# Kernel optimization log

Hardware: AMD Instinct MI355X
Metric: run time of the kernel (lower is better)

The kernel has to match this reference:

```python
import jax, jax.numpy as jnp
import numpy as np

N_NODES = 20000
N_EDGES = 256000
DIM = 128
N_LAYERS = 4


def _bn(x, gamma, beta, eps=1e-5):
    # BatchNorm1d in training mode: batch statistics over the node/edge axis
    mu = x.mean(0)
    var = ((x - mu) ** 2).mean(0)
    return gamma * (x - mu) * jax.lax.rsqrt(var + eps) + beta


def setup_inputs() -> dict:
    key = jax.random.key(0)
    ks = jax.random.split(key, 32)
    s = 1.0 / np.sqrt(DIM)
    inp = {
        'h': jax.random.normal(ks[0], (N_NODES, DIM), jnp.float32),
        'e': jax.random.normal(ks[1], (N_EDGES, DIM), jnp.float32),
        'src': jax.random.randint(ks[2], (N_EDGES,), 0, N_NODES, jnp.int32),
        'dst': jax.random.randint(ks[3], (N_EDGES,), 0, N_NODES, jnp.int32),
        'W_emb_h': jax.random.normal(ks[4], (DIM, DIM), jnp.float32) * s,
        'b_emb_h': jnp.zeros((DIM,), jnp.float32),
        'W_emb_e': jax.random.normal(ks[5], (DIM, DIM), jnp.float32) * s,
        'b_emb_e': jnp.zeros((DIM,), jnp.float32),
    }
    for i, nm in enumerate(['A', 'B', 'C', 'D', 'E']):
        inp[nm + 'w'] = jax.random.normal(ks[6 + i], (N_LAYERS, DIM, DIM), jnp.float32) * s
        inp[nm + 'b'] = jnp.zeros((N_LAYERS, DIM), jnp.float32)
    inp['gh'] = jnp.ones((N_LAYERS, DIM), jnp.float32)
    inp['bh'] = jnp.zeros((N_LAYERS, DIM), jnp.float32)
    inp['ge'] = jnp.ones((N_LAYERS, DIM), jnp.float32)
    inp['be'] = jnp.zeros((N_LAYERS, DIM), jnp.float32)
    return inp


def reference(h, e, src, dst, W_emb_h, b_emb_h, W_emb_e, b_emb_e,
              Aw, Ab, Bw, Bb, Cw, Cb, Dw, Db, Ew, Eb, gh, bh, ge, be):
    n_nodes = h.shape[0]
    # input embeddings
    h = h @ W_emb_h + b_emb_h
    e = e @ W_emb_e + b_emb_e
    for l in range(Aw.shape[0]):
        h_in, e_in = h, e
        Ah = h @ Aw[l] + Ab[l]
        Bh = h @ Bw[l] + Bb[l]
        Dh = h @ Dw[l] + Db[l]
        Eh = h @ Ew[l] + Eb[l]
        Ce = e @ Cw[l] + Cb[l]
        # edge gates: e_ij = D h_i + E h_j + C e_ij  (edge i->j)
        e_new = Dh[src] + Eh[dst] + Ce            # [E, D]
        sigma = jax.nn.sigmoid(e_new)
        num = jax.ops.segment_sum(sigma * Bh[src], dst, num_segments=n_nodes)
        den = jax.ops.segment_sum(sigma, dst, num_segments=n_nodes)
        h_new = Ah + num / (den + 1e-6)
        h_new = _bn(h_new, gh[l], bh[l])
        e_new = _bn(e_new, ge[l], be[l])
        # relu + residual (dropout = 0)
        h = h_in + jax.nn.relu(h_new)
        e = e_in + jax.nn.relu(e_new)
    return h
```

## Files before the change

kernel.cpp:

```cpp
#include <hip/hip_runtime.h>
#include <hip/hip_bf16.h>

typedef __attribute__((ext_vector_type(8))) short short8;
typedef __attribute__((ext_vector_type(4))) float floatx4;
typedef __attribute__((ext_vector_type(4))) unsigned short ushortx4;

__device__ __forceinline__ float bf2f(unsigned short u) {
    union { float f; unsigned int i; } v; v.i = ((unsigned int)u) << 16; return v.f;
}
__device__ __forceinline__ unsigned short f2bf(float f) {
    union { float f; unsigned int i; } v; v.f = f;
    unsigned int r = v.i + 0x7fffu + ((v.i >> 16) & 1u);
    return (unsigned short)(r >> 16);
}

__global__ void deg_count(const int* __restrict__ dst, int* __restrict__ deg, int E) {
    int i = blockIdx.x * 256 + threadIdx.x;
    if (i < E) atomicAdd(&deg[dst[i]], 1);
}

__global__ __launch_bounds__(1024) void scan_rowptr(const int* __restrict__ deg,
                                                    int* __restrict__ rowptr,
                                                    int* __restrict__ cursor, int N) {
    const int CH = 20;
    __shared__ int buf[1024];
    int t = threadIdx.x;
    int base = t * CH;
    int local[CH];
    int tot = 0;
#pragma unroll
    for (int k = 0; k < CH; ++k) {
        int i = base + k;
        int v = (i < N) ? deg[i] : 0;
        local[k] = tot;
        tot += v;
    }
    buf[t] = tot;
    __syncthreads();
    for (int off = 1; off < 1024; off <<= 1) {
        int x = (t >= off) ? buf[t - off] : 0;
        __syncthreads();
        buf[t] += x;
        __syncthreads();
    }
    int excl = buf[t] - tot;
#pragma unroll
    for (int k = 0; k < CH; ++k) {
        int i = base + k;
        if (i < N) { rowptr[i] = excl + local[k]; cursor[i] = excl + local[k]; }
    }
    if (t == 1023) rowptr[N] = buf[1023];
}

__global__ void scatter_edges(const int* __restrict__ src, const int* __restrict__ dst,
                              int* __restrict__ cursor, int* __restrict__ eix,
                              int* __restrict__ sx, int E) {
    int i = blockIdx.x * 256 + threadIdx.x;
    if (i >= E) return;
    int d = dst[i];
    int pos = atomicAdd(&cursor[d], 1);
    eix[pos] = i;
    sx[pos] = src[i];
}

__global__ void transpose_w(const float* __restrict__ Wh,
                            const float* __restrict__ We,
                            const float* __restrict__ Aw,
                            const float* __restrict__ Bw,
                            const float* __restrict__ Cw,
                            const float* __restrict__ Dw,
                            const float* __restrict__ Ew,
                            unsigned short* __restrict__ Wt) {
    int i = blockIdx.x * 256 + threadIdx.x;
    const int total = 22 * 16384;
    if (i >= total) return;
    int slot = i >> 14;
    int r = i & 16383;
    int n = r >> 7;
    int k = r & 127;
    const float* srcp;
    if (slot == 0) srcp = Wh;
    else if (slot == 1) srcp = We;
    else {
        int t = slot - 2;
        int l = t / 5, w = t % 5;
        const float* bases[5] = {Aw, Bw, Cw, Dw, Ew};
        srcp = bases[w] + l * 16384;
    }
    Wt[i] = f2bf(srcp[k * 128 + n]);
}

template <int IN_BF16, int OUT_BF16, int GATHER>
__global__ __launch_bounds__(256) void gemm128(const void* __restrict__ Ain,
                                               const int* __restrict__ ridx,
                                               const unsigned short* __restrict__ Wt,
                                               const float* __restrict__ bias,
                                               void* __restrict__ Cout, int nStrips) {
    const int lane = threadIdx.x & 63;
    const int wv = threadIdx.x >> 6;
    const int m16 = lane & 15;
    const int kg = lane >> 4;

    short8 b[4][2];
#pragma unroll
    for (int j = 0; j < 2; ++j)
#pragma unroll
        for (int ks = 0; ks < 4; ++ks)
            b[ks][j] = *(const short8*)(Wt + ((wv * 2 + j) * 16 + m16) * 128 + ks * 32 + kg * 8);

    floatx4 bv[2];
#pragma unroll
    for (int j = 0; j < 2; ++j)
        bv[j] = *(const floatx4*)(bias + (wv * 2 + j) * 16 + kg * 4);

    const float* Af = (const float*)Ain;
    const unsigned short* Ab16 = (const unsigned short*)Ain;

    const int stride = gridDim.x;
    int s0 = blockIdx.x;
    if (s0 >= nStrips) return;

    auto loadA = [&](int s, short8* a) {
        int rowA = s * 16 + m16;
        if (GATHER) rowA = ridx[rowA];
        size_t rowBase = (size_t)rowA * 128;
#pragma unroll
        for (int ks = 0; ks < 4; ++ks) {
            int off = ks * 32 + kg * 8;
            if (IN_BF16) {
                a[ks] = *(const short8*)(Ab16 + rowBase + off);
            } else {
                floatx4 f0 = *(const floatx4*)(Af + rowBase + off);
                floatx4 f1 = *(const floatx4*)(Af + rowBase + off + 4);
                short8 t;
                t[0] = (short)f2bf(f0[0]); t[1] = (short)f2bf(f0[1]);
                t[2] = (short)f2bf(f0[2]); t[3] = (short)f2bf(f0[3]);
                t[4] = (short)f2bf(f1[0]); t[5] = (short)f2bf(f1[1]);
                t[6] = (short)f2bf(f1[2]); t[7] = (short)f2bf(f1[3]);
                a[ks] = t;
            }
        }
    };

    short8 a0[4], a1[4];
    loadA(s0, a0);
    for (int s = s0; s < nStrips; s += stride) {
        int sn = s + stride;
        if (sn < nStrips) loadA(sn, a1);

        floatx4 acc[2];
        acc[0] = (floatx4){0.f, 0.f, 0.f, 0.f};
        acc[1] = (floatx4){0.f, 0.f, 0.f, 0.f};
#pragma unroll
        for (int ks = 0; ks < 4; ++ks) {
            acc[0] = __builtin_amdgcn_mfma_f32_16x16x32_bf16(b[ks][0], a0[ks], acc[0], 0, 0, 0);
            acc[1] = __builtin_amdgcn_mfma_f32_16x16x32_bf16(b[ks][1], a0[ks], acc[1], 0, 0, 0);
        }

        size_t rbase = ((size_t)s * 16 + m16) * 128;
#pragma unroll
        for (int j = 0; j < 2; ++j) {
            int c0 = (wv * 2 + j) * 16 + kg * 4;
            if (OUT_BF16) {
                ushortx4 o;
#pragma unroll
                for (int i = 0; i < 4; ++i) o[i] = f2bf(acc[j][i] + bv[j][i]);
                *(ushortx4*)((unsigned short*)Cout + rbase + c0) = o;
            } else {
                floatx4 o;
#pragma unroll
                for (int i = 0; i < 4; ++i) o[i] = acc[j][i] + bv[j][i];
                *(floatx4*)((float*)Cout + rbase + c0) = o;
            }
        }
#pragma unroll
        for (int ks = 0; ks < 4; ++ks) a0[ks] = a1[ks];
    }
}

__global__ __launch_bounds__(1024) void gemm_h4(const float* __restrict__ h_cur,
                                                const unsigned short* __restrict__ WtL,
                                                const float* __restrict__ Abi,
                                                const float* __restrict__ Bbi,
                                                const float* __restrict__ Dbi,
                                                const float* __restrict__ Ebi,
                                                float* __restrict__ AhB,
                                                unsigned short* __restrict__ BD16,
                                                unsigned short* __restrict__ Eh16,
                                                int nStrips) {
    const int lane = threadIdx.x & 63;
    const int w = threadIdx.x >> 6;
    const int m16 = lane & 15;
    const int kg = lane >> 4;

    short8 bf[4][2];
    floatx4 bv[2];
    if (w < 8) {
        const int slot = (w < 4) ? 0 : 4;
        const float* bp = (w < 4) ? Abi : Ebi;
        const int ntb = (w & 3) * 2;
#pragma unroll
        for (int j = 0; j < 2; ++j) {
#pragma unroll
            for (int ks = 0; ks < 4; ++ks)
                bf[ks][j] = *(const short8*)(WtL + slot * 16384 +
                                             ((ntb + j) * 16 + m16) * 128 + ks * 32 + kg * 8);
            bv[j] = *(const floatx4*)(bp + (ntb + j) * 16 + kg * 4);
        }
    } else {
        const int nt = w - 8;
#pragma unroll
        for (int ks = 0; ks < 4; ++ks) {
            bf[ks][0] = *(const short8*)(WtL + 1 * 16384 + (nt * 16 + m16) * 128 + ks * 32 + kg * 8);
            bf[ks][1] = *(const short8*)(WtL + 3 * 16384 + (nt * 16 + m16) * 128 + ks * 32 + kg * 8);
        }
        bv[0] = *(const floatx4*)(Bbi + nt * 16 + kg * 4);
        bv[1] = *(const floatx4*)(Dbi + nt * 16 + kg * 4);
    }

    for (int s = blockIdx.x; s < nStrips; s += gridDim.x) {
        size_t rowBase = ((size_t)s * 16 + m16) * 128;
        short8 a[4];
#pragma unroll
        for (int ks = 0; ks < 4; ++ks) {
            int off = ks * 32 + kg * 8;
            floatx4 f0 = *(const floatx4*)(h_cur + rowBase + off);
            floatx4 f1 = *(const floatx4*)(h_cur + rowBase + off + 4);
            short8 t;
            t[0] = (short)f2bf(f0[0]); t[1] = (short)f2bf(f0[1]);
            t[2] = (short)f2bf(f0[2]); t[3] = (short)f2bf(f0[3]);
            t[4] = (short)f2bf(f1[0]); t[5] = (short)f2bf(f1[1]);
            t[6] = (short)f2bf(f1[2]); t[7] = (short)f2bf(f1[3]);
            a[ks] = t;
        }

        floatx4 acc0 = (floatx4){0.f, 0.f, 0.f, 0.f};
        floatx4 acc1 = (floatx4){0.f, 0.f, 0.f, 0.f};
#pragma unroll
        for (int ks = 0; ks < 4; ++ks) {
            acc0 = __builtin_amdgcn_mfma_f32_16x16x32_bf16(bf[ks][0], a[ks], acc0, 0, 0, 0);
            acc1 = __builtin_amdgcn_mfma_f32_16x16x32_bf16(bf[ks][1], a[ks], acc1, 0, 0, 0);
        }

        size_t r = (size_t)s * 16 + m16;
        if (w < 4) {
            const int ntb = (w & 3) * 2;
            floatx4 o0, o1;
#pragma unroll
            for (int i = 0; i < 4; ++i) { o0[i] = acc0[i] + bv[0][i]; o1[i] = acc1[i] + bv[1][i]; }
            *(floatx4*)(AhB + r * 128 + (ntb + 0) * 16 + kg * 4) = o0;
            *(floatx4*)(AhB + r * 128 + (ntb + 1) * 16 + kg * 4) = o1;
        } else if (w < 8) {
            const int ntb = (w & 3) * 2;
            ushortx4 o0, o1;
#pragma unroll
            for (int i = 0; i < 4; ++i) {
                o0[i] = f2bf(acc0[i] + bv[0][i]);
                o1[i] = f2bf(acc1[i] + bv[1][i]);
            }
            *(ushortx4*)(Eh16 + r * 128 + (ntb + 0) * 16 + kg * 4) = o0;
            *(ushortx4*)(Eh16 + r * 128 + (ntb + 1) * 16 + kg * 4) = o1;
        } else {
            const int nt = w - 8;
            short8 o;
#pragma unroll
            for (int i = 0; i < 4; ++i) {
                o[2 * i]     = (short)f2bf(acc0[i] + bv[0][i]);
                o[2 * i + 1] = (short)f2bf(acc1[i] + bv[1][i]);
            }
            *(short8*)(BD16 + r * 256 + (nt * 16 + kg * 4) * 2) = o;
        }
    }
}

template <int DO_E>
__global__ __launch_bounds__(256) void node_aggregate(unsigned short* __restrict__ Ce,
                                                      const unsigned short* __restrict__ BD16,
                                                      const unsigned short* __restrict__ Eh16,
                                                      const int* __restrict__ rowptr,
                                                      const int* __restrict__ sx,
                                                      const float* __restrict__ Ah,
                                                      float* __restrict__ h_new,
                                                      float* __restrict__ sums, int N) {
    const int q = threadIdx.x & 31;
    const int g = threadIdx.x >> 5;
    float hs[4] = {0.f, 0.f, 0.f, 0.f};
    float hq[4] = {0.f, 0.f, 0.f, 0.f};
    float es[4] = {0.f, 0.f, 0.f, 0.f};
    float eq[4] = {0.f, 0.f, 0.f, 0.f};
    for (int d = blockIdx.x * 8 + g; d < N; d += gridDim.x * 8) {
        int beg = rowptr[d], end = rowptr[d + 1];
        ushortx4 eh4 = *(const ushortx4*)(Eh16 + (size_t)d * 128 + q * 4);
        float ehf[4];
#pragma unroll
        for (int k = 0; k < 4; ++k) ehf[k] = bf2f(eh4[k]);
        float num[4] = {0.f, 0.f, 0.f, 0.f};
        float den[4] = {0.f, 0.f, 0.f, 0.f};
        int j = beg;
        for (; j + 1 < end; j += 2) {
            int s0 = sx[j], s1 = sx[j + 1];
            ushortx4 c0 = *(const ushortx4*)(Ce + (size_t)j * 128 + q * 4);
            ushortx4 c1 = *(const ushortx4*)(Ce + (size_t)(j + 1) * 128 + q * 4);
            short8 bd0 = *(const short8*)(BD16 + (size_t)s0 * 256 + q * 8);
            short8 bd1 = *(const short8*)(BD16 + (size_t)s1 * 256 + q * 8);
            ushortx4 o0, o1;
#pragma unroll
            for (int k = 0; k < 4; ++k) {
                float en0 = bf2f(c0[k]) + bf2f((unsigned short)bd0[2 * k + 1]) + ehf[k];
                float en1 = bf2f(c1[k]) + bf2f((unsigned short)bd1[2 * k + 1]) + ehf[k];
                if (DO_E) {
                    es[k] += en0 + en1;
                    eq[k] += en0 * en0 + en1 * en1;
                    o0[k] = f2bf(en0);
                    o1[k] = f2bf(en1);
                }
                float sg0 = 1.f / (1.f + __expf(-en0));
                float sg1 = 1.f / (1.f + __expf(-en1));
                den[k] += sg0 + sg1;
                num[k] += sg0 * bf2f((unsigned short)bd0[2 * k])
                        + sg1 * bf2f((unsigned short)bd1[2 * k]);
            }
            if (DO_E) {
                *(ushortx4*)(Ce + (size_t)j * 128 + q * 4) = o0;
                *(ushortx4*)(Ce + (size_t)(j + 1) * 128 + q * 4) = o1;
            }
        }
        if (j < end) {
            int s0 = sx[j];
            ushortx4 c0 = *(const ushortx4*)(Ce + (size_t)j * 128 + q * 4);
            short8 bd0 = *(const short8*)(BD16 + (size_t)s0 * 256 + q * 8);
            ushortx4 o0;
#pragma unroll
            for (int k = 0; k < 4; ++k) {
                float en0 = bf2f(c0[k]) + bf2f((unsigned short)bd0[2 * k + 1]) + ehf[k];
                if (DO_E) {
                    es[k] += en0;
                    eq[k] += en0 * en0;
                    o0[k] = f2bf(en0);
                }
                float sg0 = 1.f / (1.f + __expf(-en0));
                den[k] += sg0;
                num[k] += sg0 * bf2f((unsigned short)bd0[2 * k]);
            }
            if (DO_E) *(ushortx4*)(Ce + (size_t)j * 128 + q * 4) = o0;
        }
        floatx4 ah = *(const floatx4*)(Ah + (size_t)d * 128 + q * 4);
        floatx4 out;
#pragma unroll
        for (int k = 0; k < 4; ++k) {
            float v = ah[k] + num[k] / (den[k] + 1e-6f);
            out[k] = v;
            hs[k] += v;
            hq[k] += v * v;
        }
        *(floatx4*)(h_new + (size_t)d * 128 + q * 4) = out;
    }
    __shared__ float ls[512];
    ls[threadIdx.x] = 0.f;
    ls[256 + threadIdx.x] = 0.f;
    __syncthreads();
#pragma unroll
    for (int k = 0; k < 4; ++k) {
        atomicAdd(&ls[q * 4 + k], hs[k]);
        atomicAdd(&ls[128 + q * 4 + k], hq[k]);
        if (DO_E) {
            atomicAdd(&ls[256 + q * 4 + k], es[k]);
            atomicAdd(&ls[384 + q * 4 + k], eq[k]);
        }
    }
    __syncthreads();
    atomicAdd(&sums[threadIdx.x], ls[threadIdx.x]);
    if (DO_E) atomicAdd(&sums[256 + threadIdx.x], ls[256 + threadIdx.x]);
}

__global__ void finalize_stats(const float* __restrict__ sums,
                               const float* __restrict__ gh,
                               const float* __restrict__ bh,
                               const float* __restrict__ ge,
                               const float* __restrict__ be,
                               float* __restrict__ coef, int N, int E) {
    int c = threadIdx.x;
    if (c >= 128) return;
    float muh = sums[c] / (float)N;
    float vh = fmaxf(sums[128 + c] / (float)N - muh * muh, 0.f);
    float rsh = rsqrtf(vh + 1e-5f);
    float g = gh[c], bt = bh[c];
    coef[c] = g * rsh;
    coef[128 + c] = bt - g * rsh * muh;
    float mue = sums[256 + c] / (float)E;
    float ve = fmaxf(sums[384 + c] / (float)E - mue * mue, 0.f);
    float rse = rsqrtf(ve + 1e-5f);
    float g2 = ge[c], b2 = be[c];
    coef[256 + c] = g2 * rse;
    coef[384 + c] = b2 - g2 * rse * mue;
}

__global__ __launch_bounds__(256) void h_update(const float* __restrict__ h_new,
                                                const float* __restrict__ coef,
                                                float* __restrict__ h_cur,
                                                float* __restrict__ out, int N) {
    const int c = threadIdx.x & 127;
    float sa = coef[c], sb = coef[128 + c];
    int total = N * 128;
    for (int i = blockIdx.x * blockDim.x + threadIdx.x; i < total; i += gridDim.x * blockDim.x) {
        float v = h_new[i] * sa + sb;
        v = v > 0.f ? v : 0.f;
        float h = h_cur[i] + v;
        h_cur[i] = h;
        if (out) out[i] = h;
    }
}

__global__ __launch_bounds__(256) void e_update(const unsigned short* __restrict__ e_new,
                                                const float* __restrict__ coef,
                                                unsigned short* __restrict__ e_cur, int E) {
    int total8 = E * 16;
    for (int idx = blockIdx.x * blockDim.x + threadIdx.x; idx < total8;
         idx += gridDim.x * blockDim.x) {
        int c8 = (idx & 15) * 8;
        short8 en = *(const short8*)(e_new + (size_t)idx * 8);
        short8 ec = *(const short8*)(e_cur + (size_t)idx * 8);
        floatx4 sa0 = *(const floatx4*)(coef + 256 + c8);
        floatx4 sa1 = *(const floatx4*)(coef + 256 + c8 + 4);
        floatx4 sb0 = *(const floatx4*)(coef + 384 + c8);
        floatx4 sb1 = *(const floatx4*)(coef + 384 + c8 + 4);
        short8 r;
#pragma unroll
        for (int k = 0; k < 8; ++k) {
            float sa = (k < 4) ? sa0[k] : sa1[k - 4];
            float sb = (k < 4) ? sb0[k] : sb1[k - 4];
            float v = bf2f((unsigned short)en[k]) * sa + sb;
            v = v > 0.f ? v : 0.f;
            r[k] = (short)f2bf(bf2f((unsigned short)ec[k]) + v);
        }
        *(short8*)(e_cur + (size_t)idx * 8) = r;
    }
}

extern "C" void kernel_launch(void* const* d_in, const int* in_sizes, int n_in,
                              void* d_out, int out_size, void* d_ws, size_t ws_size,
                              hipStream_t stream) {
    const int N = 20000, E = 256000, L = 4;

    const float* h_in = (const float*)d_in[0];
    const float* e_in = (const float*)d_in[1];
    const int* src = (const int*)d_in[2];
    const int* dst = (const int*)d_in[3];
    const float* Wemb_h = (const float*)d_in[4];
    const float* bemb_h = (const float*)d_in[5];
    const float* Wemb_e = (const float*)d_in[6];
    const float* bemb_e = (const float*)d_in[7];
    const float* Aw = (const float*)d_in[8];
    const float* Abi = (const float*)d_in[9];
    const float* Bw = (const float*)d_in[10];
    const float* Bbi = (const float*)d_in[11];
    const float* Cw = (const float*)d_in[12];
    const float* Cbi = (const float*)d_in[13];
    const float* Dw = (const float*)d_in[14];
    const float* Dbi = (const float*)d_in[15];
    const float* Ew = (const float*)d_in[16];
    const float* Ebi = (const float*)d_in[17];
    const float* gh = (const float*)d_in[18];
    const float* bh = (const float*)d_in[19];
    const float* ge = (const float*)d_in[20];
    const float* be = (const float*)d_in[21];

    char* p = (char*)d_ws;
    auto carve = [&](size_t bytes) {
        void* r = (void*)p;
        p += ((bytes + 255) & ~(size_t)255);
        return r;
    };
    unsigned short* Wt = (unsigned short*)carve((size_t)22 * 16384 * 2);
    float* h_cur = (float*)carve((size_t)N * 128 * 4);
    unsigned short* e_cur = (unsigned short*)carve((size_t)E * 128 * 2);
    unsigned short* e_new = (unsigned short*)carve((size_t)E * 128 * 2);
    float* AhB = (float*)carve((size_t)N * 128 * 4);
    unsigned short* BD16 = (unsigned short*)carve((size_t)N * 256 * 2);
    unsigned short* Eh16 = (unsigned short*)carve((size_t)N * 128 * 2);
    float* h_newB = (float*)carve((size_t)N * 128 * 4);
    float* sums = (float*)carve(4 * 128 * 4);
    float* coef = (float*)carve(4 * 128 * 4);
    int* deg = (int*)carve((size_t)N * 4);
    int* rowptr = (int*)carve((size_t)(N + 1) * 4);
    int* cursor = (int*)carve((size_t)N * 4);
    int* eix = (int*)carve((size_t)E * 4);
    int* sx = (int*)carve((size_t)E * 4);

    hipMemsetAsync(deg, 0, (size_t)N * 4, stream);
    deg_count<<<(E + 255) / 256, 256, 0, stream>>>(dst, deg, E);
    scan_rowptr<<<1, 1024, 0, stream>>>(deg, rowptr, cursor, N);
    scatter_edges<<<(E + 255) / 256, 256, 0, stream>>>(src, dst, cursor, eix, sx, E);

    transpose_w<<<(22 * 16384 + 255) / 256, 256, 0, stream>>>(Wemb_h, Wemb_e, Aw, Bw, Cw, Dw, Ew, Wt);

    gemm128<0, 0, 0><<<1024, 256, 0, stream>>>(h_in, nullptr, Wt + 0 * 16384, bemb_h, h_cur, N / 16);
    gemm128<0, 1, 1><<<1024, 256, 0, stream>>>(e_in, eix, Wt + 1 * 16384, bemb_e, e_cur, E / 16);

    for (int l = 0; l < L; ++l) {
        int last = (l == L - 1);
        hipMemsetAsync(sums, 0, 4 * 128 * 4, stream);
        const unsigned short* WtL = Wt + (size_t)(2 + l * 5) * 16384;
        gemm_h4<<<250, 1024, 0, stream>>>(h_cur, WtL, Abi + l * 128, Bbi + l * 128,
                                          Dbi + l * 128, Ebi + l * 128, AhB, BD16, Eh16,
                                          N / 16);
        gemm128<1, 1, 0><<<1024, 256, 0, stream>>>(e_cur, nullptr, WtL + 2 * 16384, Cbi + l * 128,
                                                   e_new, E / 16);
        if (!last)
            node_aggregate<1><<<1250, 256, 0, stream>>>(e_new, BD16, Eh16, rowptr, sx, AhB,
                                                        h_newB, sums, N);
        else
            node_aggregate<0><<<1250, 256, 0, stream>>>(e_new, BD16, Eh16, rowptr, sx, AhB,
                                                        h_newB, sums, N);
        finalize_stats<<<1, 128, 0, stream>>>(sums, gh + l * 128, bh + l * 128, ge + l * 128,
                                              be + l * 128, coef, N, E);
        h_update<<<512, 256, 0, stream>>>(h_newB, coef, h_cur, last ? (float*)d_out : nullptr, N);
        if (!last) e_update<<<2048, 256, 0, stream>>>(e_new, coef, e_cur, E);
    }
}
```

Before: 1.061 ms.

## Stage GEMM A tiles into LDS via async global_load_lds double buffering

```diff
diff --git a/kernel.cpp b/kernel.cpp
--- a/kernel.cpp
+++ b/kernel.cpp
@@ -4,6 +4,9 @@
 typedef __attribute__((ext_vector_type(8))) short short8;
 typedef __attribute__((ext_vector_type(4))) float floatx4;
 typedef __attribute__((ext_vector_type(4))) unsigned short ushortx4;
+
+typedef __attribute__((address_space(3))) unsigned int lds_u32;
+typedef __attribute__((address_space(1))) const unsigned int g_u32;
 
 __device__ __forceinline__ float bf2f(unsigned short u) {
     union { float f; unsigned int i; } v; v.i = ((unsigned int)u) << 16; return v.f;
@@ -90,12 +93,20 @@
     Wt[i] = f2bf(srcp[k * 128 + n]);
 }
 
-template <int IN_BF16, int OUT_BF16, int GATHER>
-__global__ __launch_bounds__(256) void gemm128(const void* __restrict__ Ain,
-                                               const int* __restrict__ ridx,
-                                               const unsigned short* __restrict__ Wt,
-                                               const float* __restrict__ bias,
-                                               void* __restrict__ Cout, int nStrips) {
+template <int IN_F32, int OUT_BF16, int GATHER>
+__global__ __launch_bounds__(256) void gemm_lds(const void* __restrict__ Ain,
+                                                const int* __restrict__ ridx,
+                                                const unsigned short* __restrict__ Wt,
+                                                const float* __restrict__ bias,
+                                                void* __restrict__ Cout,
+                                                int nTiles, int Mrows) {
+    constexpr int ROWB = IN_F32 ? 512 : 256;
+    constexpr int RSH = IN_F32 ? 9 : 8;
+    constexpr int TILEB = 64 * ROWB;
+    constexpr int PERW = TILEB / 4;
+    constexpr int ROUNDS = PERW / 1024;
+    __shared__ unsigned char smem[2][TILEB];
+
     const int lane = threadIdx.x & 63;
     const int wv = threadIdx.x >> 6;
     const int m16 = lane & 15;
@@ -107,74 +118,93 @@
 #pragma unroll
         for (int ks = 0; ks < 4; ++ks)
             b[ks][j] = *(const short8*)(Wt + ((wv * 2 + j) * 16 + m16) * 128 + ks * 32 + kg * 8);
-
     floatx4 bv[2];
 #pragma unroll
     for (int j = 0; j < 2; ++j)
         bv[j] = *(const floatx4*)(bias + (wv * 2 + j) * 16 + kg * 4);
 
-    const float* Af = (const float*)Ain;
-    const unsigned short* Ab16 = (const unsigned short*)Ain;
-
-    const int stride = gridDim.x;
-    int s0 = blockIdx.x;
-    if (s0 >= nStrips) return;
-
-    auto loadA = [&](int s, short8* a) {
-        int rowA = s * 16 + m16;
-        if (GATHER) rowA = ridx[rowA];
-        size_t rowBase = (size_t)rowA * 128;
-#pragma unroll
-        for (int ks = 0; ks < 4; ++ks) {
-            int off = ks * 32 + kg * 8;
-            if (IN_BF16) {
-                a[ks] = *(const short8*)(Ab16 + rowBase + off);
-            } else {
-                floatx4 f0 = *(const floatx4*)(Af + rowBase + off);
-                floatx4 f1 = *(const floatx4*)(Af + rowBase + off + 4);
-                short8 t;
-                t[0] = (short)f2bf(f0[0]); t[1] = (short)f2bf(f0[1]);
-                t[2] = (short)f2bf(f0[2]); t[3] = (short)f2bf(f0[3]);
-                t[4] = (short)f2bf(f1[0]); t[5] = (short)f2bf(f1[1]);
-                t[6] = (short)f2bf(f1[2]); t[7] = (short)f2bf(f1[3]);
-                a[ks] = t;
-            }
+    const unsigned char* Ab = (const unsigned char*)Ain;
+
+    int t0 = blockIdx.x;
+    if (t0 >= nTiles) return;
+
+    auto stage = [&](int bufsel, int t) {
+#pragma unroll
+        for (int r = 0; r < ROUNDS; ++r) {
+            int d = wv * PERW + r * 1024 + lane * 16;
+            int row = d >> RSH;
+            int scol;
+            if (IN_F32)
+                scol = (d ^ ((row & 3) << 5)) & (ROWB - 1);
+            else
+                scol = (d ^ ((row & 7) << 4)) & (ROWB - 1);
+            int grow = t * 64 + row;
+            grow = grow < Mrows ? grow : Mrows - 1;
+            if (GATHER) grow = ridx[grow];
+            const unsigned char* gp = Ab + (size_t)grow * ROWB + scol;
+            unsigned char* lp = &smem[bufsel][wv * PERW + r * 1024];
+            __builtin_amdgcn_global_load_lds((g_u32*)gp, (lds_u32*)lp, 16, 0, 0);
         }
     };
 
-    short8 a0[4], a1[4];
-    loadA(s0, a0);
-    for (int s = s0; s < nStrips; s += stride) {
-        int sn = s + stride;
-        if (sn < nStrips) loadA(sn, a1);
-
-        floatx4 acc[2];
-        acc[0] = (floatx4){0.f, 0.f, 0.f, 0.f};
-        acc[1] = (floatx4){0.f, 0.f, 0.f, 0.f};
-#pragma unroll
-        for (int ks = 0; ks < 4; ++ks) {
-            acc[0] = __builtin_amdgcn_mfma_f32_16x16x32_bf16(b[ks][0], a0[ks], acc[0], 0, 0, 0);
-            acc[1] = __builtin_amdgcn_mfma_f32_16x16x32_bf16(b[ks][1], a0[ks], acc[1], 0, 0, 0);
-        }
-
-        size_t rbase = ((size_t)s * 16 + m16) * 128;
-#pragma unroll
-        for (int j = 0; j < 2; ++j) {
-            int c0 = (wv * 2 + j) * 16 + kg * 4;
-            if (OUT_BF16) {
-                ushortx4 o;
-#pragma unroll
-                for (int i = 0; i < 4; ++i) o[i] = f2bf(acc[j][i] + bv[j][i]);
-                *(ushortx4*)((unsigned short*)Cout + rbase + c0) = o;
-            } else {
-                floatx4 o;
-#pragma unroll
-                for (int i = 0; i < 4; ++i) o[i] = acc[j][i] + bv[j][i];
-                *(floatx4*)((float*)Cout + rbase + c0) = o;
-            }
-        }
-#pragma unroll
-        for (int ks = 0; ks < 4; ++ks) a0[ks] = a1[ks];
+    int cur = 0;
+    stage(0, t0);
+    __syncthreads();
+
+    for (int t = t0; t < nTiles; t += gridDim.x) {
+        int tn = t + gridDim.x;
+        if (tn < nTiles) stage(cur ^ 1, tn);
+
+        const unsigned char* sb = smem[cur];
+#pragma unroll
+        for (int st = 0; st < 4; ++st) {
+            short8 a[4];
+#pragma unroll
+            for (int ks = 0; ks < 4; ++ks) {
+                if (IN_F32) {
+                    int aoff = (st * 16 + m16) * 512 + ks * 128 + kg * 32;
+                    aoff ^= (m16 & 3) << 5;
+                    floatx4 f0 = *(const floatx4*)(sb + aoff);
+                    floatx4 f1 = *(const floatx4*)(sb + aoff + 16);
+                    short8 tt;
+                    tt[0] = (short)f2bf(f0[0]); tt[1] = (short)f2bf(f0[1]);
+                    tt[2] = (short)f2bf(f0[2]); tt[3] = (short)f2bf(f0[3]);
+                    tt[4] = (short)f2bf(f1[0]); tt[5] = (short)f2bf(f1[1]);
+                    tt[6] = (short)f2bf(f1[2]); tt[7] = (short)f2bf(f1[3]);
+                    a[ks] = tt;
+                } else {
+                    int aoff = (st * 16 + m16) * 256 + ks * 64 + kg * 16;
+                    aoff ^= (m16 & 7) << 4;
+                    a[ks] = *(const short8*)(sb + aoff);
+                }
+            }
+            floatx4 acc0 = (floatx4){0.f, 0.f, 0.f, 0.f};
+            floatx4 acc1 = (floatx4){0.f, 0.f, 0.f, 0.f};
+#pragma unroll
+            for (int ks = 0; ks < 4; ++ks) {
+                acc0 = __builtin_amdgcn_mfma_f32_16x16x32_bf16(b[ks][0], a[ks], acc0, 0, 0, 0);
+                acc1 = __builtin_amdgcn_mfma_f32_16x16x32_bf16(b[ks][1], a[ks], acc1, 0, 0, 0);
+            }
+            size_t row = (size_t)t * 64 + st * 16 + m16;
+#pragma unroll
+            for (int j = 0; j < 2; ++j) {
+                int c0 = (wv * 2 + j) * 16 + kg * 4;
+                floatx4 accj = j ? acc1 : acc0;
+                if (OUT_BF16) {
+                    ushortx4 o;
+#pragma unroll
+                    for (int i = 0; i < 4; ++i) o[i] = f2bf(accj[i] + bv[j][i]);
+                    *(ushortx4*)((unsigned short*)Cout + row * 128 + c0) = o;
+                } else {
+                    floatx4 o;
+#pragma unroll
+                    for (int i = 0; i < 4; ++i) o[i] = accj[i] + bv[j][i];
+                    *(floatx4*)((float*)Cout + row * 128 + c0) = o;
+                }
+            }
+        }
+        __syncthreads();
+        cur ^= 1;
     }
 }
 
@@ -441,6 +471,7 @@
                               void* d_out, int out_size, void* d_ws, size_t ws_size,
                               hipStream_t stream) {
     const int N = 20000, E = 256000, L = 4;
+    const int NPAD = 20032;
 
     const float* h_in = (const float*)d_in[0];
     const float* e_in = (const float*)d_in[1];
@@ -472,7 +503,7 @@
         return r;
     };
     unsigned short* Wt = (unsigned short*)carve((size_t)22 * 16384 * 2);
-    float* h_cur = (float*)carve((size_t)N * 128 * 4);
+    float* h_cur = (float*)carve((size_t)NPAD * 128 * 4);
     unsigned short* e_cur = (unsigned short*)carve((size_t)E * 128 * 2);
     unsigned short* e_new = (unsigned short*)carve((size_t)E * 128 * 2);
     float* AhB = (float*)carve((size_t)N * 128 * 4);
@@ -494,8 +525,10 @@
 
     transpose_w<<<(22 * 16384 + 255) / 256, 256, 0, stream>>>(Wemb_h, Wemb_e, Aw, Bw, Cw, Dw, Ew, Wt);
 
-    gemm128<0, 0, 0><<<1024, 256, 0, stream>>>(h_in, nullptr, Wt + 0 * 16384, bemb_h, h_cur, N / 16);
-    gemm128<0, 1, 1><<<1024, 256, 0, stream>>>(e_in, eix, Wt + 1 * 16384, bemb_e, e_cur, E / 16);
+    gemm_lds<1, 0, 0><<<313, 256, 0, stream>>>(h_in, nullptr, Wt + 0 * 16384, bemb_h,
+                                               h_cur, 313, N);
+    gemm_lds<1, 1, 1><<<1024, 256, 0, stream>>>(e_in, eix, Wt + 1 * 16384, bemb_e,
+                                                e_cur, E / 64, E);
 
     for (int l = 0; l < L; ++l) {
         int last = (l == L - 1);
@@ -504,8 +537,8 @@
         gemm_h4<<<250, 1024, 0, stream>>>(h_cur, WtL, Abi + l * 128, Bbi + l * 128,
                                           Dbi + l * 128, Ebi + l * 128, AhB, BD16, Eh16,
                                           N / 16);
-        gemm128<1, 1, 0><<<1024, 256, 0, stream>>>(e_cur, nullptr, WtL + 2 * 16384, Cbi + l * 128,
-                                                   e_new, E / 16);
+        gemm_lds<0, 1, 0><<<1024, 256, 0, stream>>>(e_cur, nullptr, WtL + 2 * 16384,
+                                                    Cbi + l * 128, e_new, E / 64, E);
         if (!last)
             node_aggregate<1><<<1250, 256, 0, stream>>>(e_new, BD16, Eh16, rowptr, sx, AhB,
                                                         h_newB, sums, N);
```

New measurement: 967.4 us. 1.1x faster.
